# Optimization experiments

Measured on AMD Instinct MI355X. Metric: run time of the kernel, lower is better.

The kernel has to match this reference:

```python
import jax, jax.numpy as jnp
import numpy as np

N_NODES = 100000
N_EDGES = 3200000
HIDDEN = 64


def setup_inputs() -> dict:
    key = jax.random.key(0)
    ks = jax.random.split(key, 12)
    x = jax.random.normal(ks[0], (N_NODES, 4), dtype=jnp.float32)
    edge_index = jax.random.randint(ks[1], (2, N_EDGES), 0, N_NODES, dtype=jnp.int64)
    edge_attr = jax.random.normal(ks[2], (N_EDGES, 4), dtype=jnp.float32)
    W1 = jax.random.normal(ks[3], (4, HIDDEN), dtype=jnp.float32) * 0.5
    b1 = jax.random.normal(ks[4], (HIDDEN,), dtype=jnp.float32) * 0.1
    W2 = jax.random.normal(ks[5], (HIDDEN, HIDDEN), dtype=jnp.float32) * 0.125
    b2 = jax.random.normal(ks[6], (HIDDEN,), dtype=jnp.float32) * 0.1
    Wm1 = jax.random.normal(ks[7], (2 * HIDDEN + 4, HIDDEN), dtype=jnp.float32) * 0.1
    bm1 = jax.random.normal(ks[8], (HIDDEN,), dtype=jnp.float32) * 0.1
    Wm2 = jax.random.normal(ks[9], (HIDDEN, 1), dtype=jnp.float32) * 0.125
    bm2 = jax.random.normal(ks[10], (1,), dtype=jnp.float32) * 0.1
    return dict(x=x, edge_index=edge_index, edge_attr=edge_attr,
                W1=W1, b1=b1, W2=W2, b2=b2, Wm1=Wm1, bm1=bm1, Wm2=Wm2, bm2=bm2)


def _gcn_conv(x, W, b, src, dst, norm, n):
    # x' = D^{-1/2} (A + I) D^{-1/2} (x W) + b   (PyG GCNConv w/ self-loops)
    h = x @ W                                   # [N, H]
    msg = h[src] * norm[:, None]                # gather + scale  [E+N, H]
    out = jax.ops.segment_sum(msg, dst, num_segments=n)
    return out + b


def reference(x, edge_index, edge_attr, W1, b1, W2, b2, Wm1, bm1, Wm2, bm2):
    n = x.shape[0]
    src, dst = edge_index[0], edge_index[1]
    loops = jnp.arange(n, dtype=src.dtype)
    src_f = jnp.concatenate([src, loops])       # edges + self-loops
    dst_f = jnp.concatenate([dst, loops])
    deg = jax.ops.segment_sum(jnp.ones_like(src_f, dtype=x.dtype), dst_f, num_segments=n)
    dis = jnp.where(deg > 0, jax.lax.rsqrt(deg), 0.0)
    norm = dis[src_f] * dis[dst_f]              # [E+N]

    h = jax.nn.relu(_gcn_conv(x, W1, b1, src_f, dst_f, norm, n))
    h = jax.nn.relu(_gcn_conv(h, W2, b2, src_f, dst_f, norm, n))

    # per-edge gather + concat + 2-layer MLP -> scalar logit per edge
    edge_in = jnp.concatenate([h[src], h[dst], edge_attr], axis=1)  # [E, 2H+4]
    z = jax.nn.relu(edge_in @ Wm1 + bm1)
    logits = (z @ Wm2 + bm2)[:, 0]
    return logits
```

## Files before the change

kernel.cpp:

```cpp
#include <hip/hip_runtime.h>
#include <hip/hip_fp16.h>


#define HDIM 64
#define NBK 2048


__global__ void __launch_bounds__(256) hist_k(const int* __restrict__ dst,
                                              int* __restrict__ bucketCnt,
                                              int E, int CH) {
    __shared__ int hist[NBK];
    int t = threadIdx.x;
    for (int b = t; b < NBK; b += 256) hist[b] = 0;
    __syncthreads();
    int rs = blockIdx.x * CH, re = min(E, rs + CH);
    for (int e = rs + t; e < re; e += 256) atomicAdd(&hist[dst[e] >> 6], 1);
    __syncthreads();
    for (int b = t; b < NBK; b += 256) {
        int h = hist[b];
        if (h) atomicAdd(&bucketCnt[b], h);
    }
}

__global__ void bscan_k(const int* __restrict__ cnt, int* __restrict__ base,
                        int* __restrict__ cur, int E) {
    __shared__ int wtot[4];
    int t = threadIdx.x;
    int lane = t & 63, wid = t >> 6;
    int i0 = t * 8;
    int v[8]; int s = 0;
    #pragma unroll
    for (int j = 0; j < 8; j++) { v[j] = cnt[i0 + j]; s += v[j]; }
    int ws = s;
    #pragma unroll
    for (int d = 1; d < 64; d <<= 1) {
        int n = __shfl_up(ws, d, 64);
        if (lane >= d) ws += n;
    }
    if (lane == 63) wtot[wid] = ws;
    __syncthreads();
    int woff = 0;
    #pragma unroll
    for (int w = 0; w < 4; w++) if (w < wid) woff += wtot[w];
    int ex = woff + ws - s;
    #pragma unroll
    for (int j = 0; j < 8; j++) {
        base[i0 + j] = ex; cur[i0 + j] = ex;
        ex += v[j];
    }
    if (t == 255) base[NBK] = E;
}

__global__ void __launch_bounds__(256) part_k(const int* __restrict__ src,
                                              const int* __restrict__ dst,
                                              int* __restrict__ bucketCur,
                                              int2* __restrict__ pairs,
                                              int E, int CH) {
    __shared__ int hist[NBK];
    __shared__ int mybase[NBK];
    __shared__ int lcur[NBK];
    int t = threadIdx.x;
    int rs = blockIdx.x * CH, re = min(E, rs + CH);
    for (int b = t; b < NBK; b += 256) hist[b] = 0;
    __syncthreads();
    for (int e = rs + t; e < re; e += 256) atomicAdd(&hist[dst[e] >> 6], 1);
    __syncthreads();
    for (int b = t; b < NBK; b += 256) {
        int h = hist[b];
        mybase[b] = h ? atomicAdd(&bucketCur[b], h) : 0;
        lcur[b] = 0;
    }
    __syncthreads();
    for (int e = rs + t; e < re; e += 256) {
        int d = dst[e];
        int b = d >> 6;
        int o = atomicAdd(&lcur[b], 1);
        pairs[mybase[b] + o] = make_int2(src[e], d);
    }
}

__global__ void __launch_bounds__(256) csrify_k(
    const int2* __restrict__ pairs, const int* __restrict__ base,
    int* __restrict__ csrc, int* __restrict__ rowptr,
    float* __restrict__ dis, int N, int E) {
    __shared__ int cnt[64];
    __shared__ int off[64];
    int b = blockIdx.x, t = threadIdx.x;
    if (t < 64) cnt[t] = 0;
    __syncthreads();
    int rs = base[b], re = base[b + 1];
    for (int i = rs + t; i < re; i += 256) atomicAdd(&cnt[pairs[i].y & 63], 1);
    __syncthreads();
    if (t < 64) {
        int deg = cnt[t];
        int n = b * 64 + t;
        if (n < N) dis[n] = rsqrtf((float)(deg + 1));
        int val = deg;
        #pragma unroll
        for (int d = 1; d < 64; d <<= 1) {
            int up = __shfl_up(val, d, 64);
            if (t >= d) val += up;
        }
        int excl = rs + val - deg;
        off[t] = excl;
        if (n < N) rowptr[n] = excl;
    }
    if (b == 0 && t == 0) rowptr[N] = E;
    __syncthreads();
    for (int i = rs + t; i < re; i += 256) {
        int2 p = pairs[i];
        int o = atomicAdd(&off[p.y & 63], 1);
        csrc[o] = p.x;
    }
}

__global__ void xs_k(const float* __restrict__ x, const float* __restrict__ dis,
                     float* __restrict__ xs, int N) {
    int i = blockIdx.x * 256 + threadIdx.x;
    if (i >= N) return;
    float d = dis[i];
    float4 v = *(const float4*)(x + (size_t)i * 4);
    v.x *= d; v.y *= d; v.z *= d; v.w *= d;
    *(float4*)(xs + (size_t)i * 4) = v;
}

__global__ void __launch_bounds__(256) aggX_k(
    const float* __restrict__ xs, float* __restrict__ xa,
    const int* __restrict__ rowptr, const int* __restrict__ csrc,
    const float* __restrict__ dis, int N) {
    int t = threadIdx.x;
    int node = blockIdx.x * 64 + (t >> 2);
    int f = t & 3;
    if (node >= N) return;
    int beg = rowptr[node], end = rowptr[node + 1];
    float acc = 0.f;
    int e = beg;
    for (; e + 2 <= end; e += 2) {
        int c0 = csrc[e], c1 = csrc[e + 1];
        float v0 = xs[(size_t)c0 * 4 + f];
        float v1 = xs[(size_t)c1 * 4 + f];
        acc += v0; acc += v1;
    }
    if (e < end) acc += xs[(size_t)csrc[e] * 4 + f];
    float di = dis[node];
    xa[(size_t)node * 4 + f] = di * (acc + xs[(size_t)node * 4 + f]);
}

__global__ void h1_k(const float* __restrict__ xa, const float* __restrict__ W1,
                     const float* __restrict__ b1, const float* __restrict__ dis,
                     __half* __restrict__ h1s, int N) {
    int gid = blockIdx.x * 256 + threadIdx.x;
    if (gid >= N * HDIM) return;
    int i = gid >> 6, f = gid & 63;
    float4 v = *(const float4*)(xa + (size_t)i * 4);
    float acc = b1[f];
    acc = fmaf(v.x, W1[f], acc);
    acc = fmaf(v.y, W1[64 + f], acc);
    acc = fmaf(v.z, W1[128 + f], acc);
    acc = fmaf(v.w, W1[192 + f], acc);
    h1s[gid] = __float2half(dis[i] * fmaxf(acc, 0.f));
}

__global__ void __launch_bounds__(256) agg2_k(
    const __half* __restrict__ h1s, __half* __restrict__ g,
    const int* __restrict__ rowptr, const int* __restrict__ csrc,
    const float* __restrict__ dis, int N) {
    int wid = threadIdx.x >> 6, lane = threadIdx.x & 63;
    int i = blockIdx.x * 4 + wid;
    if (i >= N) return;
    int beg = rowptr[i], end = rowptr[i + 1];
    int side = lane >> 5, lh = lane & 31;
    float ax = 0.f, ay = 0.f;
    int e = beg;
    for (; e + 4 <= end; e += 4) {
        int c0 = csrc[e + side];
        int c1 = csrc[e + 2 + side];
        float2 f0 = __half22float2(*(const __half2*)(h1s + (size_t)c0 * HDIM + lh * 2));
        float2 f1 = __half22float2(*(const __half2*)(h1s + (size_t)c1 * HDIM + lh * 2));
        ax += f0.x + f1.x; ay += f0.y + f1.y;
    }
    if (e + 2 <= end) {
        int c = csrc[e + side];
        float2 f0 = __half22float2(*(const __half2*)(h1s + (size_t)c * HDIM + lh * 2));
        ax += f0.x; ay += f0.y;
        e += 2;
    }
    if (e < end && side == 0) {
        int c = csrc[e];
        float2 f0 = __half22float2(*(const __half2*)(h1s + (size_t)c * HDIM + lh * 2));
        ax += f0.x; ay += f0.y;
    }
    ax += __shfl_xor(ax, 32, 64);
    ay += __shfl_xor(ay, 32, 64);
    if (side == 0) {
        float di = dis[i];
        float2 hf = __half22float2(*(const __half2*)(h1s + (size_t)i * HDIM + lh * 2));
        ax = di * (ax + hf.x);
        ay = di * (ay + hf.y);
        *(__half2*)(g + (size_t)i * HDIM + lh * 2) = __floats2half2_rn(ax, ay);
    }
}

__global__ void gemm64b_k(const __half* __restrict__ gin, const float* __restrict__ W2,
                          const float* __restrict__ b2, float* __restrict__ h2, int N) {
    __shared__ float w[64 * 64];
    int t = threadIdx.x;
    for (int j = t; j < 64 * 64; j += 256) w[j] = W2[j];
    __syncthreads();
    int gid = blockIdx.x * 256 + t;
    if (gid >= N * HDIM) return;
    int i = gid >> 6, f = gid & 63;
    const __half2* hr = (const __half2*)(gin + (size_t)i * HDIM);
    float acc = 0.f;
    #pragma unroll 8
    for (int k = 0; k < 32; k++) {
        float2 hv = __half22float2(hr[k]);
        acc = fmaf(hv.x, w[(2 * k) * 64 + f], acc);
        acc = fmaf(hv.y, w[(2 * k + 1) * 64 + f], acc);
    }
    h2[gid] = fmaxf(acc + b2[f], 0.f);
}

__global__ void pq_k(const float* __restrict__ h, const float* __restrict__ Wm1,
                     const float* __restrict__ bm1,
                     __half* __restrict__ Ph, __half* __restrict__ Qh, int N) {
    __shared__ float w[128 * 64];
    int t = threadIdx.x;
    for (int j = t; j < 128 * 64; j += 256) w[j] = Wm1[j];
    __syncthreads();
    int gid = blockIdx.x * 256 + t;
    if (gid >= N * HDIM) return;
    int i = gid >> 6, f = gid & 63;
    const float* hr = h + (size_t)i * HDIM;
    float a = bm1[f], b = 0.f;
    #pragma unroll 8
    for (int k = 0; k < 64; k++) {
        float hv = hr[k];
        a = fmaf(hv, w[k * 64 + f], a);
        b = fmaf(hv, w[(64 + k) * 64 + f], b);
    }
    Ph[gid] = __float2half(a);
    Qh[gid] = __float2half(b);
}

__device__ __forceinline__ float mlp8(uint4 pv, uint4 qv, float4 eav,
                                      const float wer[4][8], const float w2r[8]) {
    float p = 0.f;
    #pragma unroll
    for (int w = 0; w < 4; w++) {
        unsigned pu = (&pv.x)[w], qu = (&qv.x)[w];
        float2 pf = __half22float2(__builtin_bit_cast(__half2, pu));
        float2 qf = __half22float2(__builtin_bit_cast(__half2, qu));
        int j0 = 2 * w, j1 = 2 * w + 1;
        float z0 = pf.x + qf.x;
        z0 = fmaf(eav.x, wer[0][j0], z0); z0 = fmaf(eav.y, wer[1][j0], z0);
        z0 = fmaf(eav.z, wer[2][j0], z0); z0 = fmaf(eav.w, wer[3][j0], z0);
        float z1 = pf.y + qf.y;
        z1 = fmaf(eav.x, wer[0][j1], z1); z1 = fmaf(eav.y, wer[1][j1], z1);
        z1 = fmaf(eav.z, wer[2][j1], z1); z1 = fmaf(eav.w, wer[3][j1], z1);
        p = fmaf(fmaxf(z0, 0.f), w2r[j0], p);
        p = fmaf(fmaxf(z1, 0.f), w2r[j1], p);
    }
    return p;
}

__global__ void __launch_bounds__(256) edgefin_k(
    const int* __restrict__ src, const int* __restrict__ dst,
    const float* __restrict__ ea,
    const __half* __restrict__ Ph, const __half* __restrict__ Qh,
    const float* __restrict__ Wm1, const float* __restrict__ Wm2,
    const float* __restrict__ bm2, float* __restrict__ out, int E) {
    int q = threadIdx.x & 7;
    int fb = q * 8;
    float w2r[8];
    float wer[4][8];
    *(float4*)&w2r[0] = *(const float4*)(Wm2 + fb);
    *(float4*)&w2r[4] = *(const float4*)(Wm2 + fb + 4);
    #pragma unroll
    for (int r = 0; r < 4; r++) {
        *(float4*)&wer[r][0] = *(const float4*)(Wm1 + (128 + r) * 64 + fb);
        *(float4*)&wer[r][4] = *(const float4*)(Wm1 + (128 + r) * 64 + fb + 4);
    }
    float b2v = bm2[0];

    int base = blockIdx.x * 64 + (threadIdx.x >> 3);
    int gstride = gridDim.x * 64;
    for (int e1 = base; e1 < E; e1 += gstride) {
        int e2 = e1 + 32; int e2c = (e2 < E) ? e2 : (E - 1);
        int s1 = src[e1], d1 = dst[e1];
        int s2 = src[e2c], d2 = dst[e2c];
        uint4 pv1 = *(const uint4*)((const unsigned short*)Ph + (size_t)s1 * HDIM + fb);
        uint4 qv1 = *(const uint4*)((const unsigned short*)Qh + (size_t)d1 * HDIM + fb);
        uint4 pv2 = *(const uint4*)((const unsigned short*)Ph + (size_t)s2 * HDIM + fb);
        uint4 qv2 = *(const uint4*)((const unsigned short*)Qh + (size_t)d2 * HDIM + fb);
        float4 ea1 = *(const float4*)(ea + (size_t)e1 * 4);
        float4 ea2 = *(const float4*)(ea + (size_t)e2c * 4);
        float p1 = mlp8(pv1, qv1, ea1, wer, w2r);
        float p2 = mlp8(pv2, qv2, ea2, wer, w2r);
        p1 += __shfl_xor(p1, 1, 64); p1 += __shfl_xor(p1, 2, 64); p1 += __shfl_xor(p1, 4, 64);
        p2 += __shfl_xor(p2, 1, 64); p2 += __shfl_xor(p2, 2, 64); p2 += __shfl_xor(p2, 4, 64);
        if (q == 0) {
            out[e1] = p1 + b2v;
            if (e2 < E) out[e2] = p2 + b2v;
        }
    }
}

extern "C" void kernel_launch(void* const* d_in, const int* in_sizes, int n_in,
                              void* d_out, int out_size, void* d_ws, size_t ws_size,
                              hipStream_t stream) {
    const float* x   = (const float*)d_in[0];
    const int*   ei  = (const int*)d_in[1];
    const float* ea  = (const float*)d_in[2];
    const float* W1  = (const float*)d_in[3];
    const float* b1  = (const float*)d_in[4];
    const float* W2  = (const float*)d_in[5];
    const float* b2  = (const float*)d_in[6];
    const float* Wm1 = (const float*)d_in[7];
    const float* bm1 = (const float*)d_in[8];
    const float* Wm2 = (const float*)d_in[9];
    const float* bm2 = (const float*)d_in[10];
    float* out = (float*)d_out;

    int N = in_sizes[0] / 4;
    int E = in_sizes[1] / 2;
    const int* src = ei;
    const int* dst = ei + E;
    int nbuck = (N + 63) >> 6;

    char* wp = (char*)d_ws;
    auto carve = [&](size_t bytes) -> void* {
        void* p = (void*)wp;
        wp += (bytes + 255) & ~(size_t)255;
        return p;
    };
    int*   bucketCnt  = (int*)carve(NBK * 4);
    int*   bucketBase = (int*)carve((NBK + 1) * 4);
    int*   bucketCur  = (int*)carve(NBK * 4);
    float* dis        = (float*)carve((size_t)N * 4);
    int*   rowptr     = (int*)carve((size_t)(N + 1) * 4);
    int*   csrc       = (int*)carve((size_t)E * 4);
    int2*  pairs      = (int2*)carve((size_t)E * 8);
    float* xs         = (float*)carve((size_t)N * 4 * sizeof(float));
    float* xa         = (float*)carve((size_t)N * 4 * sizeof(float));
    __half* S2        = (__half*)carve((size_t)N * HDIM * 2);
    __half* S3        = (__half*)carve((size_t)N * HDIM * 2);
    float*  h2 = (float*)pairs;
    __half* h1s = S2;
    __half* g   = S3;
    __half* Ph  = S3;
    __half* Qh  = S2;

    hipMemsetAsync(bucketCnt, 0, NBK * 4, stream);

    int CH = (E + 511) / 512;

    hist_k<<<512, 256, 0, stream>>>(dst, bucketCnt, E, CH);
    bscan_k<<<1, 256, 0, stream>>>(bucketCnt, bucketBase, bucketCur, E);
    part_k<<<512, 256, 0, stream>>>(src, dst, bucketCur, pairs, E, CH);
    csrify_k<<<nbuck, 256, 0, stream>>>(pairs, bucketBase, csrc, rowptr, dis, N, E);
    xs_k<<<(N + 255) / 256, 256, 0, stream>>>(x, dis, xs, N);
    aggX_k<<<(N + 63) / 64, 256, 0, stream>>>(xs, xa, rowptr, csrc, dis, N);
    h1_k<<<(N * HDIM + 255) / 256, 256, 0, stream>>>(xa, W1, b1, dis, h1s, N);
    agg2_k<<<(N + 3) / 4, 256, 0, stream>>>(h1s, g, rowptr, csrc, dis, N);
    gemm64b_k<<<(N * HDIM + 255) / 256, 256, 0, stream>>>(g, W2, b2, h2, N);
    pq_k<<<(N * HDIM + 255) / 256, 256, 0, stream>>>(h2, Wm1, bm1, Ph, Qh, N);
    edgefin_k<<<2048, 256, 0, stream>>>(src, dst, ea, Ph, Qh, Wm1, Wm2, bm2, out, E);
}
```

Measured before the change: 676.1 us.

## Fuse W2 GEMM with P/Q projection; widen agg2 gathers; 4-way edge ILP

New measurement: 616.9 us. -8.8%, faster.

```diff
diff --git a/kernel.cpp b/kernel.cpp
--- a/kernel.cpp
+++ b/kernel.cpp
@@ -161,6 +161,14 @@
     h1s[gid] = __float2half(dis[i] * fmaxf(acc, 0.f));
 }
 
+__device__ __forceinline__ void acc4(const __half* __restrict__ p,
+                                     float& a0, float& a1, float& a2, float& a3) {
+    uint2 u = *(const uint2*)p;
+    float2 f01 = __half22float2(__builtin_bit_cast(__half2, u.x));
+    float2 f23 = __half22float2(__builtin_bit_cast(__half2, u.y));
+    a0 += f01.x; a1 += f01.y; a2 += f23.x; a3 += f23.y;
+}
+
 __global__ void __launch_bounds__(256) agg2_k(
     const __half* __restrict__ h1s, __half* __restrict__ g,
     const int* __restrict__ rowptr, const int* __restrict__ csrc,
@@ -169,78 +177,76 @@
     int i = blockIdx.x * 4 + wid;
     if (i >= N) return;
     int beg = rowptr[i], end = rowptr[i + 1];
-    int side = lane >> 5, lh = lane & 31;
-    float ax = 0.f, ay = 0.f;
+    int rid = lane >> 4, lh = lane & 15;
+    float a0 = 0.f, a1 = 0.f, a2 = 0.f, a3 = 0.f;
     int e = beg;
-    for (; e + 4 <= end; e += 4) {
-        int c0 = csrc[e + side];
-        int c1 = csrc[e + 2 + side];
-        float2 f0 = __half22float2(*(const __half2*)(h1s + (size_t)c0 * HDIM + lh * 2));
-        float2 f1 = __half22float2(*(const __half2*)(h1s + (size_t)c1 * HDIM + lh * 2));
-        ax += f0.x + f1.x; ay += f0.y + f1.y;
-    }
-    if (e + 2 <= end) {
-        int c = csrc[e + side];
-        float2 f0 = __half22float2(*(const __half2*)(h1s + (size_t)c * HDIM + lh * 2));
-        ax += f0.x; ay += f0.y;
-        e += 2;
-    }
-    if (e < end && side == 0) {
-        int c = csrc[e];
-        float2 f0 = __half22float2(*(const __half2*)(h1s + (size_t)c * HDIM + lh * 2));
-        ax += f0.x; ay += f0.y;
-    }
-    ax += __shfl_xor(ax, 32, 64);
-    ay += __shfl_xor(ay, 32, 64);
-    if (side == 0) {
+    for (; e + 8 <= end; e += 8) {
+        int c0 = csrc[e + rid];
+        int c1 = csrc[e + 4 + rid];
+        acc4(h1s + (size_t)c0 * HDIM + lh * 4, a0, a1, a2, a3);
+        acc4(h1s + (size_t)c1 * HDIM + lh * 4, a0, a1, a2, a3);
+    }
+    if (e + 4 <= end) {
+        int c = csrc[e + rid];
+        acc4(h1s + (size_t)c * HDIM + lh * 4, a0, a1, a2, a3);
+        e += 4;
+    }
+    int rem = end - e;
+    if (rid < rem) {
+        int c = csrc[e + rid];
+        acc4(h1s + (size_t)c * HDIM + lh * 4, a0, a1, a2, a3);
+    }
+    a0 += __shfl_xor(a0, 16, 64); a0 += __shfl_xor(a0, 32, 64);
+    a1 += __shfl_xor(a1, 16, 64); a1 += __shfl_xor(a1, 32, 64);
+    a2 += __shfl_xor(a2, 16, 64); a2 += __shfl_xor(a2, 32, 64);
+    a3 += __shfl_xor(a3, 16, 64); a3 += __shfl_xor(a3, 32, 64);
+    if (rid == 0) {
         float di = dis[i];
-        float2 hf = __half22float2(*(const __half2*)(h1s + (size_t)i * HDIM + lh * 2));
-        ax = di * (ax + hf.x);
-        ay = di * (ay + hf.y);
-        *(__half2*)(g + (size_t)i * HDIM + lh * 2) = __floats2half2_rn(ax, ay);
-    }
-}
-
-__global__ void gemm64b_k(const __half* __restrict__ gin, const float* __restrict__ W2,
-                          const float* __restrict__ b2, float* __restrict__ h2, int N) {
-    __shared__ float w[64 * 64];
-    int t = threadIdx.x;
-    for (int j = t; j < 64 * 64; j += 256) w[j] = W2[j];
-    __syncthreads();
-    int gid = blockIdx.x * 256 + t;
-    if (gid >= N * HDIM) return;
-    int i = gid >> 6, f = gid & 63;
-    const __half2* hr = (const __half2*)(gin + (size_t)i * HDIM);
-    float acc = 0.f;
-    #pragma unroll 8
-    for (int k = 0; k < 32; k++) {
-        float2 hv = __half22float2(hr[k]);
-        acc = fmaf(hv.x, w[(2 * k) * 64 + f], acc);
-        acc = fmaf(hv.y, w[(2 * k + 1) * 64 + f], acc);
-    }
-    h2[gid] = fmaxf(acc + b2[f], 0.f);
-}
-
-__global__ void pq_k(const float* __restrict__ h, const float* __restrict__ Wm1,
-                     const float* __restrict__ bm1,
-                     __half* __restrict__ Ph, __half* __restrict__ Qh, int N) {
-    __shared__ float w[128 * 64];
-    int t = threadIdx.x;
-    for (int j = t; j < 128 * 64; j += 256) w[j] = Wm1[j];
-    __syncthreads();
-    int gid = blockIdx.x * 256 + t;
-    if (gid >= N * HDIM) return;
-    int i = gid >> 6, f = gid & 63;
-    const float* hr = h + (size_t)i * HDIM;
-    float a = bm1[f], b = 0.f;
-    #pragma unroll 8
-    for (int k = 0; k < 64; k++) {
-        float hv = hr[k];
-        a = fmaf(hv, w[k * 64 + f], a);
-        b = fmaf(hv, w[(64 + k) * 64 + f], b);
-    }
-    Ph[gid] = __float2half(a);
-    Qh[gid] = __float2half(b);
+        uint2 u = *(const uint2*)(h1s + (size_t)i * HDIM + lh * 4);
+        float2 s01 = __half22float2(__builtin_bit_cast(__half2, u.x));
+        float2 s23 = __half22float2(__builtin_bit_cast(__half2, u.y));
+        a0 = di * (a0 + s01.x); a1 = di * (a1 + s01.y);
+        a2 = di * (a2 + s23.x); a3 = di * (a3 + s23.y);
+        uint2 o;
+        o.x = __builtin_bit_cast(unsigned, __floats2half2_rn(a0, a1));
+        o.y = __builtin_bit_cast(unsigned, __floats2half2_rn(a2, a3));
+        *(uint2*)(g + (size_t)i * HDIM + lh * 4) = o;
+    }
+}
+
+__global__ void __launch_bounds__(256) pqfuse_k(
+    const __half* __restrict__ g, const float* __restrict__ W2,
+    const float* __restrict__ b2, const float* __restrict__ Wm1,
+    const float* __restrict__ bm1,
+    __half* __restrict__ Ph, __half* __restrict__ Qh, int N) {
+    __shared__ float w2[64 * 64];
+    __shared__ float wm[128 * 64];
+    int t = threadIdx.x;
+    for (int j = t; j < 64 * 64; j += 256) w2[j] = W2[j];
+    for (int j = t; j < 128 * 64; j += 256) wm[j] = Wm1[j];
+    __syncthreads();
+    int wave = t >> 6, f = t & 63;
+    float b2v = b2[f], bm1v = bm1[f];
+    for (int i = blockIdx.x * 4 + wave; i < N; i += gridDim.x * 4) {
+        const __half2* hr = (const __half2*)(g + (size_t)i * HDIM);
+        float acc = 0.f;
+        #pragma unroll 8
+        for (int k = 0; k < 32; k++) {
+            float2 hv = __half22float2(hr[k]);
+            acc = fmaf(hv.x, w2[(2 * k) * 64 + f], acc);
+            acc = fmaf(hv.y, w2[(2 * k + 1) * 64 + f], acc);
+        }
+        float h2v = fmaxf(acc + b2v, 0.f);
+        float a = bm1v, b = 0.f;
+        #pragma unroll 8
+        for (int k = 0; k < 64; k++) {
+            float hk = __shfl(h2v, k, 64);
+            a = fmaf(hk, wm[k * 64 + f], a);
+            b = fmaf(hk, wm[(64 + k) * 64 + f], b);
+        }
+        Ph[(size_t)i * HDIM + f] = __float2half(a);
+        Qh[(size_t)i * HDIM + f] = __float2half(b);
+    }
 }
 
 __device__ __forceinline__ float mlp8(uint4 pv, uint4 qv, float4 eav,
@@ -283,25 +289,39 @@
     }
     float b2v = bm2[0];
 
-    int base = blockIdx.x * 64 + (threadIdx.x >> 3);
-    int gstride = gridDim.x * 64;
+    int base = blockIdx.x * 128 + (threadIdx.x >> 3);
+    int gstride = gridDim.x * 128;
     for (int e1 = base; e1 < E; e1 += gstride) {
-        int e2 = e1 + 32; int e2c = (e2 < E) ? e2 : (E - 1);
-        int s1 = src[e1], d1 = dst[e1];
-        int s2 = src[e2c], d2 = dst[e2c];
-        uint4 pv1 = *(const uint4*)((const unsigned short*)Ph + (size_t)s1 * HDIM + fb);
-        uint4 qv1 = *(const uint4*)((const unsigned short*)Qh + (size_t)d1 * HDIM + fb);
-        uint4 pv2 = *(const uint4*)((const unsigned short*)Ph + (size_t)s2 * HDIM + fb);
-        uint4 qv2 = *(const uint4*)((const unsigned short*)Qh + (size_t)d2 * HDIM + fb);
-        float4 ea1 = *(const float4*)(ea + (size_t)e1 * 4);
-        float4 ea2 = *(const float4*)(ea + (size_t)e2c * 4);
-        float p1 = mlp8(pv1, qv1, ea1, wer, w2r);
-        float p2 = mlp8(pv2, qv2, ea2, wer, w2r);
-        p1 += __shfl_xor(p1, 1, 64); p1 += __shfl_xor(p1, 2, 64); p1 += __shfl_xor(p1, 4, 64);
-        p2 += __shfl_xor(p2, 1, 64); p2 += __shfl_xor(p2, 2, 64); p2 += __shfl_xor(p2, 4, 64);
+        int ec[4];
+        uint4 pv[4], qv[4];
+        float4 eav[4];
+        #pragma unroll
+        for (int j = 0; j < 4; j++) {
+            int e = e1 + j * 32;
+            ec[j] = (e < E) ? e : (E - 1);
+        }
+        #pragma unroll
+        for (int j = 0; j < 4; j++) {
+            int s = src[ec[j]], d = dst[ec[j]];
+            pv[j] = *(const uint4*)((const unsigned short*)Ph + (size_t)s * HDIM + fb);
+            qv[j] = *(const uint4*)((const unsigned short*)Qh + (size_t)d * HDIM + fb);
+            eav[j] = *(const float4*)(ea + (size_t)ec[j] * 4);
+        }
+        float p[4];
+        #pragma unroll
+        for (int j = 0; j < 4; j++) p[j] = mlp8(pv[j], qv[j], eav[j], wer, w2r);
+        #pragma unroll
+        for (int j = 0; j < 4; j++) {
+            p[j] += __shfl_xor(p[j], 1, 64);
+            p[j] += __shfl_xor(p[j], 2, 64);
+            p[j] += __shfl_xor(p[j], 4, 64);
+        }
         if (q == 0) {
-            out[e1] = p1 + b2v;
-            if (e2 < E) out[e2] = p2 + b2v;
+            #pragma unroll
+            for (int j = 0; j < 4; j++) {
+                int e = e1 + j * 32;
+                if (e < E) out[e] = p[j] + b2v;
+            }
         }
     }
 }
@@ -345,10 +365,9 @@
     float* xa         = (float*)carve((size_t)N * 4 * sizeof(float));
     __half* S2        = (__half*)carve((size_t)N * HDIM * 2);
     __half* S3        = (__half*)carve((size_t)N * HDIM * 2);
-    float*  h2 = (float*)pairs;
     __half* h1s = S2;
     __half* g   = S3;
-    __half* Ph  = S3;
+    __half* Ph  = (__half*)pairs;
     __half* Qh  = S2;
 
     hipMemsetAsync(bucketCnt, 0, NBK * 4, stream);
@@ -363,7 +382,6 @@
     aggX_k<<<(N + 63) / 64, 256, 0, stream>>>(xs, xa, rowptr, csrc, dis, N);
     h1_k<<<(N * HDIM + 255) / 256, 256, 0, stream>>>(xa, W1, b1, dis, h1s, N);
     agg2_k<<<(N + 3) / 4, 256, 0, stream>>>(h1s, g, rowptr, csrc, dis, N);
-    gemm64b_k<<<(N * HDIM + 255) / 256, 256, 0, stream>>>(g, W2, b2, h2, N);
-    pq_k<<<(N * HDIM + 255) / 256, 256, 0, stream>>>(h2, Wm1, bm1, Ph, Qh, N);
+    pqfuse_k<<<512, 256, 0, stream>>>(g, W2, b2, Wm1, bm1, Ph, Qh, N);
     edgefin_k<<<2048, 256, 0, stream>>>(src, dst, ea, Ph, Qh, Wm1, Wm2, bm2, out, E);
 }
```
